# Kernel tuning notes

Measured on AMD Instinct MI355X. Metric: run time of the kernel, lower is better.

Reference implementation:

```python
import jax, jax.numpy as jnp
import numpy as np
import math

B, T, D, H = 4, 2048, 1024, 16
HD = D // H  # head dim = 64

def setup_inputs() -> dict:
    key = jax.random.key(0)
    ks = jax.random.split(key, 4)
    scale = 1.0 / math.sqrt(D)
    return {
        "x": jax.random.normal(ks[0], (B, T, D), dtype=jnp.float32),
        "Wq": jax.random.normal(ks[1], (D, D), dtype=jnp.float32) * scale,
        "bq": jnp.zeros((D,), dtype=jnp.float32),
        "Wk": jax.random.normal(ks[2], (D, D), dtype=jnp.float32) * scale,
        "bk": jnp.zeros((D,), dtype=jnp.float32),
        "Wv": jax.random.normal(ks[3], (D, D), dtype=jnp.float32) * scale,
        "bv": jnp.zeros((D,), dtype=jnp.float32),
    }

def reference(x, Wq, bq, Wk, bk, Wv, bv):
    b, t, d = x.shape
    # QKV projections (nn.Dense): x @ W + b
    q = x @ Wq + bq
    k = x @ Wk + bk
    v = x @ Wv + bv
    # b n (h d) -> b h n d
    def split_heads(y):
        return y.reshape(b, t, H, HD).transpose(0, 2, 1, 3)
    q, k, v = split_heads(q), split_heads(k), split_heads(v)
    # scaled dot-product attention; scale by sqrt(features // heads)
    scores = jnp.einsum("bhqd,bhkd->bhqk", q, k) / math.sqrt(HD)
    attn = jax.nn.softmax(scores, axis=-1)
    # dropout rate 0.0 / eval mode => identity
    out = jnp.einsum("bhqk,bhkd->bhqd", attn, v)
    # b h n d -> b n (h d)
    return out.transpose(0, 2, 1, 3).reshape(b, t, d)
```

## Files before the change

### kernel.cpp

```cpp
#include <hip/hip_runtime.h>
#include <math.h>

typedef unsigned short u16;
typedef short short8 __attribute__((ext_vector_type(8)));
typedef short short4v __attribute__((ext_vector_type(4)));
typedef u16 u16x4 __attribute__((ext_vector_type(4)));
typedef float f32x4 __attribute__((ext_vector_type(4)));
typedef __bf16 bf16x8 __attribute__((ext_vector_type(8)));
typedef __bf16 bf16x4 __attribute__((ext_vector_type(4)));

#define B_ 4
#define T_ 2048
#define D_ 1024
#define H_ 16
#define HD_ 64
#define BT_ 8192

__device__ __forceinline__ u16 f2bf(float f) {
  unsigned u = __builtin_bit_cast(unsigned, f);
  u = u + 0x7fffu + ((u >> 16) & 1u);
  return (u16)(u >> 16);
}
__device__ __forceinline__ f32x4 mfma16(short8 a, short8 b, f32x4 c) {
  return __builtin_amdgcn_mfma_f32_16x16x32_bf16(
      __builtin_bit_cast(bf16x8, a), __builtin_bit_cast(bf16x8, b), c, 0, 0, 0);
}
#if __has_builtin(__builtin_amdgcn_mfma_f32_16x16x16bf16_1k)
__device__ __forceinline__ f32x4 mfma_pv(short4v p, short4v v, f32x4 c) {
  return __builtin_amdgcn_mfma_f32_16x16x16bf16_1k(
      __builtin_bit_cast(bf16x4, p), __builtin_bit_cast(bf16x4, v), c, 0, 0, 0);
}
#else
__device__ __forceinline__ f32x4 mfma_pv(short4v p, short4v v, f32x4 c) {
  short8 a = {p[0], p[1], p[2], p[3], 0, 0, 0, 0};
  short8 b = {v[0], v[1], v[2], v[3], 0, 0, 0, 0};
  return mfma16(a, b, c);
}
#endif
__device__ __forceinline__ void async16(u16* lds, const u16* g) {
  __builtin_amdgcn_global_load_lds(
      (const __attribute__((address_space(1))) unsigned int*)g,
      (__attribute__((address_space(3))) unsigned int*)lds, 16, 0, 0);
}
__device__ __forceinline__ short4v pack4(float p0, float p1, float p2, float p3) {
  bf16x4 t = {(__bf16)p0, (__bf16)p1, (__bf16)p2, (__bf16)p3};
  return __builtin_bit_cast(short4v, t);
}

__global__ __launch_bounds__(256) void convert_x(const float* __restrict__ in,
                                                 u16* __restrict__ out) {
  int i = (blockIdx.x * 256 + threadIdx.x) * 4;
  float4 v = *(const float4*)&in[i];
  u16x4 o = {f2bf(v.x), f2bf(v.y), f2bf(v.z), f2bf(v.w)};
  *(u16x4*)&out[i] = o;
}

__global__ __launch_bounds__(256) void transposeW3(
    const float* __restrict__ Wq, const float* __restrict__ Wk,
    const float* __restrict__ Wv, u16* __restrict__ wtq, u16* __restrict__ wtk,
    u16* __restrict__ wtv) {
  __shared__ float sh[32][33];
  const int wsel = blockIdx.y >> 5;
  const float* in = (wsel == 0) ? Wq : (wsel == 1) ? Wk : Wv;
  u16* out = (wsel == 0) ? wtq : (wsel == 1) ? wtk : wtv;
  const int bx = blockIdx.x * 32, by = (blockIdx.y & 31) * 32;
  const int col = threadIdx.x & 31, r8 = threadIdx.x >> 5;
#pragma unroll
  for (int i = 0; i < 4; i++) {
    int row = r8 + i * 8;
    sh[row][col] = in[(size_t)(by + row) * 1024 + bx + col];
  }
  __syncthreads();
#pragma unroll
  for (int i = 0; i < 4; i++) {
    int row = r8 + i * 8;
    out[(size_t)(bx + row) * 1024 + by + col] = f2bf(sh[col][row]);
  }
}

__global__ __launch_bounds__(256, 3) void gemm_qkv3(
    const u16* __restrict__ xbf, const u16* __restrict__ wtq,
    const u16* __restrict__ wtk, const u16* __restrict__ wtv,
    const float* __restrict__ bq, const float* __restrict__ bk,
    const float* __restrict__ bv, u16* __restrict__ qh, u16* __restrict__ kh,
    u16* __restrict__ vth, float qscale) {
  __shared__ __align__(16) u16 Rs[128 * 64];
  __shared__ __align__(16) u16 Cs[128 * 64];
  const int proj = blockIdx.y >> 3;
  const int fy = blockIdx.y & 7;
  const u16* Rm;
  const u16* Cm;
  const float* bias;
  u16* out;
  float scale;
  int r0, c0, vmode;
  if (proj == 0) {
    Rm = wtq; Cm = xbf; bias = bq; out = qh; scale = qscale; vmode = 0;
    r0 = fy * 128; c0 = blockIdx.x * 128;
  } else if (proj == 1) {
    Rm = wtk; Cm = xbf; bias = bk; out = kh; scale = 1.0f; vmode = 0;
    r0 = fy * 128; c0 = blockIdx.x * 128;
  } else {
    Rm = xbf; Cm = wtv; bias = bv; out = vth; scale = 1.0f; vmode = 1;
    r0 = blockIdx.x * 128; c0 = fy * 128;
  }
  const int tid = threadIdx.x;
  const int lane = tid & 63;
  const int w = tid >> 6;
  const int wr = w >> 1, wc = w & 1;
  const int c = lane & 15, q4 = lane >> 4;
  const int cx7 = c & 7;

  f32x4 acc[4][4];
#pragma unroll
  for (int i = 0; i < 4; i++)
#pragma unroll
    for (int j = 0; j < 4; j++) {
      f32x4 z = {0.f, 0.f, 0.f, 0.f};
      acc[i][j] = z;
    }

  const int sr = tid >> 3, pc = tid & 7;

  for (int kk = 0; kk < 1024; kk += 64) {
    __syncthreads();
#pragma unroll
    for (int i = 0; i < 4; i++) {
      int row = i * 32 + sr;
      int sc = (pc ^ (row & 7)) * 8;
      async16(&Rs[(i * 256 + tid) * 8], &Rm[(size_t)(r0 + row) * 1024 + kk + sc]);
      async16(&Cs[(i * 256 + tid) * 8], &Cm[(size_t)(c0 + row) * 1024 + kk + sc]);
    }
    __syncthreads();
#pragma unroll
    for (int h = 0; h < 2; h++) {
      short8 rF[4], cF[4];
      const int ko = ((h * 4 + q4) ^ cx7) * 8;
#pragma unroll
      for (int i = 0; i < 4; i++)
        rF[i] = *(const short8*)&Rs[(wr * 64 + i * 16 + c) * 64 + ko];
#pragma unroll
      for (int j = 0; j < 4; j++)
        cF[j] = *(const short8*)&Cs[(wc * 64 + j * 16 + c) * 64 + ko];
#pragma unroll
      for (int i = 0; i < 4; i++)
#pragma unroll
        for (int j = 0; j < 4; j++) acc[i][j] = mfma16(rF[i], cF[j], acc[i][j]);
    }
  }

  if (vmode == 0) {
#pragma unroll
    for (int i = 0; i < 4; i++) {
      int ng = r0 + wr * 64 + i * 16 + q4 * 4;
      int h = ng >> 6, hd = ng & 63;
#pragma unroll
      for (int j = 0; j < 4; j++) {
        int tg = c0 + wc * 64 + j * 16 + c;
        int b = tg >> 11, tt = tg & 2047;
        u16x4 o;
#pragma unroll
        for (int r = 0; r < 4; r++)
          o[r] = f2bf((acc[i][j][r] + bias[ng + r]) * scale);
        *(u16x4*)&out[(((size_t)(b * 16 + h) * 2048 + tt) << 6) + hd] = o;
      }
    }
  } else {
#pragma unroll
    for (int i = 0; i < 4; i++) {
      int tg = r0 + wr * 64 + i * 16 + q4 * 4;
      int b = tg >> 11, tt = tg & 2047;
#pragma unroll
      for (int j = 0; j < 4; j++) {
        int ng = c0 + wc * 64 + j * 16 + c;
        int h = ng >> 6, hd = ng & 63;
        float bb = bias[ng];
        u16x4 o;
#pragma unroll
        for (int r = 0; r < 4; r++) o[r] = f2bf(acc[i][j][r] + bb);
        *(u16x4*)&out[((size_t)((b * 16 + h) * 64 + hd)) * 2048 + tt] = o;
      }
    }
  }
}

__global__ __launch_bounds__(256, 4) void attn_fused(const u16* __restrict__ Qh,
                                                     const u16* __restrict__ Kh,
                                                     const u16* __restrict__ VTh,
                                                     float* __restrict__ out) {
  __shared__ __align__(16) u16 Ks[2][64 * 64];
  __shared__ __align__(16) u16 VTs[2][64 * 64];
  const int tid = threadIdx.x;
  const int w = tid >> 6, lane = tid & 63;
  const int c = lane & 15, q4 = lane >> 4;
  const int cx7 = c & 7;
  const int qt = blockIdx.x, bh = blockIdx.y;

  short8 qf[2][2];
#pragma unroll
  for (int nblk = 0; nblk < 2; nblk++) {
    const u16* Qp =
        Qh + ((size_t)bh * T_ + qt * 128 + w * 32 + nblk * 16 + c) * 64;
    qf[nblk][0] = *(const short8*)&Qp[q4 * 8];
    qf[nblk][1] = *(const short8*)&Qp[32 + q4 * 8];
  }

  const u16* Kb = Kh + (size_t)bh * T_ * 64;
  const u16* Vb = VTh + (size_t)bh * 64 * T_;

  f32x4 O[2][4];
#pragma unroll
  for (int nblk = 0; nblk < 2; nblk++)
#pragma unroll
    for (int nb = 0; nb < 4; nb++) {
      f32x4 z = {0.f, 0.f, 0.f, 0.f};
      O[nblk][nb] = z;
    }
  float lsum[2] = {0.f, 0.f};

  const int sr = tid >> 3, pc = tid & 7;

#pragma unroll
  for (int i = 0; i < 2; i++) {
    int r = i * 32 + sr;
    int sc = (pc ^ (r & 7)) * 8;
    async16(&Ks[0][(i * 256 + tid) * 8], &Kb[(size_t)r * 64 + sc]);
    async16(&VTs[0][(i * 256 + tid) * 8], &Vb[(size_t)r * T_ + sc]);
  }

  for (int it = 0; it < T_ / 64; it++) {
    const int cur = it & 1;
    __syncthreads();
    if (it + 1 < T_ / 64) {
      const int kt = (it + 1) * 64;
#pragma unroll
      for (int i = 0; i < 2; i++) {
        int r = i * 32 + sr;
        int sc = (pc ^ (r & 7)) * 8;
        async16(&Ks[cur ^ 1][(i * 256 + tid) * 8],
                &Kb[(size_t)(kt + r) * 64 + sc]);
        async16(&VTs[cur ^ 1][(i * 256 + tid) * 8],
                &Vb[(size_t)r * T_ + kt + sc]);
      }
    }

    f32x4 S[4][2];
#pragma unroll
    for (int kb = 0; kb < 4; kb++) {
      short8 k0 =
          *(const short8*)&Ks[cur][(kb * 16 + c) * 64 + ((q4 ^ cx7) * 8)];
      short8 k1 =
          *(const short8*)&Ks[cur][(kb * 16 + c) * 64 + (((4 + q4) ^ cx7) * 8)];
#pragma unroll
      for (int nblk = 0; nblk < 2; nblk++) {
        f32x4 z = {0.f, 0.f, 0.f, 0.f};
        S[kb][nblk] = mfma16(k0, qf[nblk][0], z);
        S[kb][nblk] = mfma16(k1, qf[nblk][1], S[kb][nblk]);
      }
    }

    short4v pf[2][4];
#pragma unroll
    for (int nblk = 0; nblk < 2; nblk++) {
      float rs = 0.f;
#pragma unroll
      for (int kb = 0; kb < 4; kb++) {
        float p0 = __builtin_amdgcn_exp2f(S[kb][nblk][0]);
        float p1 = __builtin_amdgcn_exp2f(S[kb][nblk][1]);
        float p2 = __builtin_amdgcn_exp2f(S[kb][nblk][2]);
        float p3 = __builtin_amdgcn_exp2f(S[kb][nblk][3]);
        rs += (p0 + p1) + (p2 + p3);
        pf[nblk][kb] = pack4(p0, p1, p2, p3);
      }
      lsum[nblk] += rs;
    }

#pragma unroll
    for (int kb = 0; kb < 4; kb++) {
      int pch = ((kb * 2 + (q4 >> 1)) ^ cx7) * 8 + (q4 & 1) * 4;
#pragma unroll
      for (int nb = 0; nb < 4; nb++) {
        short4v vf = *(const short4v*)&VTs[cur][(nb * 16 + c) * 64 + pch];
        O[0][nb] = mfma_pv(pf[0][kb], vf, O[0][nb]);
        O[1][nb] = mfma_pv(pf[1][kb], vf, O[1][nb]);
      }
    }
  }

#pragma unroll
  for (int nblk = 0; nblk < 2; nblk++) {
    lsum[nblk] += __shfl_xor(lsum[nblk], 16);
    lsum[nblk] += __shfl_xor(lsum[nblk], 32);
  }

  const int bq = bh >> 4, h = bh & 15;
#pragma unroll
  for (int nblk = 0; nblk < 2; nblk++)
#pragma unroll
    for (int r = 0; r < 4; r++) {
      float rl = 1.0f / __shfl(lsum[nblk], q4 * 4 + r);
      int t = qt * 128 + w * 32 + nblk * 16 + q4 * 4 + r;
#pragma unroll
      for (int nb = 0; nb < 4; nb++)
        out[((size_t)(bq * T_ + t)) * 1024 + h * 64 + nb * 16 + c] =
            O[nblk][nb][r] * rl;
    }
}

extern "C" void kernel_launch(void* const* d_in, const int* in_sizes, int n_in,
                              void* d_out, int out_size, void* d_ws, size_t ws_size,
                              hipStream_t stream) {
  (void)in_sizes; (void)n_in; (void)out_size; (void)ws_size;
  const float* x  = (const float*)d_in[0];
  const float* Wq = (const float*)d_in[1];
  const float* bq = (const float*)d_in[2];
  const float* Wk = (const float*)d_in[3];
  const float* bk = (const float*)d_in[4];
  const float* Wv = (const float*)d_in[5];
  const float* bv = (const float*)d_in[6];
  float* out = (float*)d_out;

  u16* ob  = (u16*)d_out;
  u16* xbf = ob;
  u16* wtq = ob + (size_t)BT_ * D_;
  u16* wtk = wtq + (size_t)D_ * D_;
  u16* wtv = wtk + (size_t)D_ * D_;

  u16* ws  = (u16*)d_ws;
  u16* qh  = ws;
  u16* kh  = qh + (size_t)BT_ * D_;
  u16* vth = kh + (size_t)BT_ * D_;

  convert_x<<<8192, 256, 0, stream>>>(x, xbf);
  transposeW3<<<dim3(32, 96), 256, 0, stream>>>(Wq, Wk, Wv, wtq, wtk, wtv);

  const float qscale = 0.125f * 1.44269504088896f;
  gemm_qkv3<<<dim3(64, 24), 256, 0, stream>>>(xbf, wtq, wtk, wtv, bq, bk, bv,
                                              qh, kh, vth, qscale);

  attn_fused<<<dim3(16, 64), 256, 0, stream>>>(qh, kh, vth, out);
}
```

Measured before the change: 246.8 us.

## Double-buffer QKV GEMM shared tiles with K-step 32 and async prefetch

The QKV projection GEMM now uses two shared-memory buffers of 128x32 per operand instead of one 128x64 buffer. The next K slice is prefetched asynchronously while MFMAs run on the current one, cutting the barriers per step from two to one. The XOR swizzle is adapted to the narrower 32-element rows. The aim is to hide global-to-LDS load latency behind compute. The cost is twice as many loop iterations and barriers over K, with less MFMA work between them.

```diff
diff --git a/kernel.cpp b/kernel.cpp
--- a/kernel.cpp
+++ b/kernel.cpp
@@ -84,8 +84,8 @@
     const float* __restrict__ bq, const float* __restrict__ bk,
     const float* __restrict__ bv, u16* __restrict__ qh, u16* __restrict__ kh,
     u16* __restrict__ vth, float qscale) {
-  __shared__ __align__(16) u16 Rs[128 * 64];
-  __shared__ __align__(16) u16 Cs[128 * 64];
+  __shared__ __align__(16) u16 Rs[2][128 * 32];
+  __shared__ __align__(16) u16 Cs[2][128 * 32];
   const int proj = blockIdx.y >> 3;
   const int fy = blockIdx.y & 7;
   const u16* Rm;
@@ -109,7 +109,7 @@
   const int w = tid >> 6;
   const int wr = w >> 1, wc = w & 1;
   const int c = lane & 15, q4 = lane >> 4;
-  const int cx7 = c & 7;
+  const int csw = (c >> 1) & 3;
 
   f32x4 acc[4][4];
 #pragma unroll
@@ -120,33 +120,44 @@
       acc[i][j] = z;
     }
 
-  const int sr = tid >> 3, pc = tid & 7;
-
-  for (int kk = 0; kk < 1024; kk += 64) {
+  const int srow = tid >> 2, spc = tid & 3;
+
+#pragma unroll
+  for (int i = 0; i < 2; i++) {
+    int row = i * 64 + srow;
+    int sc = (spc ^ ((row >> 1) & 3)) * 8;
+    async16(&Rs[0][(i * 256 + tid) * 8], &Rm[(size_t)(r0 + row) * 1024 + sc]);
+    async16(&Cs[0][(i * 256 + tid) * 8], &Cm[(size_t)(c0 + row) * 1024 + sc]);
+  }
+
+  for (int it = 0; it < 32; it++) {
+    const int cur = it & 1;
     __syncthreads();
-#pragma unroll
-    for (int i = 0; i < 4; i++) {
-      int row = i * 32 + sr;
-      int sc = (pc ^ (row & 7)) * 8;
-      async16(&Rs[(i * 256 + tid) * 8], &Rm[(size_t)(r0 + row) * 1024 + kk + sc]);
-      async16(&Cs[(i * 256 + tid) * 8], &Cm[(size_t)(c0 + row) * 1024 + kk + sc]);
-    }
-    __syncthreads();
-#pragma unroll
-    for (int h = 0; h < 2; h++) {
-      short8 rF[4], cF[4];
-      const int ko = ((h * 4 + q4) ^ cx7) * 8;
-#pragma unroll
-      for (int i = 0; i < 4; i++)
-        rF[i] = *(const short8*)&Rs[(wr * 64 + i * 16 + c) * 64 + ko];
-#pragma unroll
-      for (int j = 0; j < 4; j++)
-        cF[j] = *(const short8*)&Cs[(wc * 64 + j * 16 + c) * 64 + ko];
-#pragma unroll
-      for (int i = 0; i < 4; i++)
-#pragma unroll
-        for (int j = 0; j < 4; j++) acc[i][j] = mfma16(rF[i], cF[j], acc[i][j]);
-    }
+    if (it + 1 < 32) {
+      const int kk = (it + 1) * 32;
+#pragma unroll
+      for (int i = 0; i < 2; i++) {
+        int row = i * 64 + srow;
+        int sc = (spc ^ ((row >> 1) & 3)) * 8;
+        async16(&Rs[cur ^ 1][(i * 256 + tid) * 8],
+                &Rm[(size_t)(r0 + row) * 1024 + kk + sc]);
+        async16(&Cs[cur ^ 1][(i * 256 + tid) * 8],
+                &Cm[(size_t)(c0 + row) * 1024 + kk + sc]);
+      }
+    }
+    short8 rF[4], cF[4];
+#pragma unroll
+    for (int i = 0; i < 4; i++)
+      rF[i] = *(const short8*)&Rs[cur][(wr * 64 + i * 16 + c) * 32 +
+                                       ((q4 ^ csw) * 8)];
+#pragma unroll
+    for (int j = 0; j < 4; j++)
+      cF[j] = *(const short8*)&Cs[cur][(wc * 64 + j * 16 + c) * 32 +
+                                       ((q4 ^ csw) * 8)];
+#pragma unroll
+    for (int i = 0; i < 4; i++)
+#pragma unroll
+      for (int j = 0; j < 4; j++) acc[i][j] = mfma16(rF[i], cF[j], acc[i][j]);
   }
 
   if (vmode == 0) {
```

Result: slower. 254.3 us (+3.0%).
